# Optimization experiments

Hardware: AMD Instinct MI355X
Metric: run time of the kernel (lower is better)

## Reference

```python
import jax, jax.numpy as jnp
import numpy as np

# Module constants from Net.__init__
KS = (3, 8, 2)          # kernel_size per pseudo-coordinate dim
K = KS[0] * KS[1] * KS[2]  # 48 spline weight matrices per layer
DIM = 3
S = 2 ** DIM            # 8 nonzero degree-1 B-spline supports per edge
MAX_RADIUS = 4.5
N, E = 20000, 500000


def _glorot(key, shape):
    fan = shape[-2] + shape[-1]
    return jax.random.normal(key, shape, jnp.float32) * jnp.sqrt(2.0 / fan)


def setup_inputs() -> dict:
    key = jax.random.key(0)
    ks = jax.random.split(key, 12)
    x = jax.random.normal(ks[0], (N, 1), jnp.float32)
    edge_index = jax.random.randint(ks[1], (2, E), 0, N)
    # raw pseudo-coordinates in [0, max_radius); normalized inside reference
    pseudo = jax.random.uniform(ks[2], (E, DIM), jnp.float32) * MAX_RADIUS
    return {
        "x": x,
        "edge_index": edge_index,
        "pseudo": pseudo,
        "W1": _glorot(ks[3], (K, 1, 32)),   "root1": _glorot(ks[4], (1, 32)),   "b1": jnp.zeros((32,), jnp.float32),
        "W2": _glorot(ks[5], (K, 32, 64)),  "root2": _glorot(ks[6], (32, 64)),  "b2": jnp.zeros((64,), jnp.float32),
        "W3": _glorot(ks[7], (K, 64, 128)), "root3": _glorot(ks[8], (64, 128)), "b3": jnp.zeros((128,), jnp.float32),
    }


def spline_basis(u):
    """Degree-1 open B-spline basis. u: [E, DIM] in [0,1].
    Returns basis [E, S] and flat kernel indices kidx [E, S] into the K weights."""
    ks_f = jnp.array(KS, jnp.float32)
    pos = u * (ks_f - 1.0)                      # [E, DIM]
    lo = jnp.floor(pos)
    frac = pos - lo                             # interpolation weight per dim
    lo_i = lo.astype(jnp.int32)
    # all 2^DIM corner offsets
    bits = jnp.array([[(s >> d) & 1 for d in range(DIM)] for s in range(S)], jnp.int32)  # [S, DIM]
    idx = jnp.clip(lo_i[:, None, :] + bits[None, :, :], 0, jnp.array(KS, jnp.int32) - 1)  # [E, S, DIM]
    w = jnp.where(bits[None, :, :] == 1, frac[:, None, :], 1.0 - frac[:, None, :])        # [E, S, DIM]
    basis = jnp.prod(w, axis=-1)                # [E, S]
    strides = jnp.array([KS[1] * KS[2], KS[2], 1], jnp.int32)
    kidx = (idx * strides[None, None, :]).sum(-1)  # [E, S]
    return basis, kidx


def spline_conv(x, src, dst, basis, kidx, W, root, bias):
    """SplineGCN layer: gather source features, weight by spline basis,
    scatter-add into per-(node, kernel) buckets, then contract with the K
    kernel matrices. Equivalent to sum_e basis * (x_src @ W[kidx]) at dst."""
    c_in = x.shape[1]
    contrib = basis[:, :, None] * x[src][:, None, :]          # [E, S, c_in]
    flat = (dst[:, None] * K + kidx).reshape(-1)              # [E*S]
    acc = jax.ops.segment_sum(contrib.reshape(-1, c_in), flat, num_segments=N * K)
    acc = acc.reshape(N, K, c_in)                             # [N, K, c_in]
    return jnp.einsum('nki,kio->no', acc, W) + x @ root + bias


def reference(x, edge_index, pseudo, W1, root1, b1, W2, root2, b2, W3, root3, b3):
    u = jnp.clip(pseudo / MAX_RADIUS, 0.0, 1.0)
    basis, kidx = spline_basis(u)
    src, dst = edge_index[0], edge_index[1]
    h = jax.nn.relu(spline_conv(x, src, dst, basis, kidx, W1, root1, b1))
    h = jax.nn.relu(spline_conv(h, src, dst, basis, kidx, W2, root2, b2))
    h = jax.nn.relu(spline_conv(h, src, dst, basis, kidx, W3, root3, b3))
    return jax.nn.log_softmax(h, axis=-1)
```

## Files before the change

### kernel.cpp

```cpp
#include <hip/hip_runtime.h>
#include <hip/hip_bf16.h>

#define NN_NODES 20000
#define NE_EDGES 500000
#define KTOT 48
#define BTSTRIDE 40

typedef __bf16 bf16x8 __attribute__((ext_vector_type(8)));
typedef float f32x4 __attribute__((ext_vector_type(4)));

__device__ inline unsigned short bf16_rne(float x) {
    unsigned int u = __float_as_uint(x);
    u = (u + 0x7fffu + ((u >> 16) & 1u)) >> 16;
    return (unsigned short)u;
}

__global__ void zero_kernel(int* __restrict__ p, int n) {
    int i = blockIdx.x * 256 + threadIdx.x;
    if (i < n) p[i] = 0;
}

__global__ void count_kernel(const int* __restrict__ ei, int* __restrict__ counts) {
    int e = blockIdx.x * 256 + threadIdx.x;
    if (e < NE_EDGES) atomicAdd(&counts[ei[NE_EDGES + e]], 1);
}

__global__ void scan_kernel(const int* __restrict__ counts, int* __restrict__ row_start) {
    __shared__ int part[256];
    const int CH = (NN_NODES + 255) / 256;
    int t = threadIdx.x;
    int begin = t * CH;
    int end = begin + CH;
    if (end > NN_NODES) end = NN_NODES;
    int sum = 0;
    for (int i = begin; i < end && i < NN_NODES; ++i) sum += counts[i];
    part[t] = sum;
    __syncthreads();
    for (int off = 1; off < 256; off <<= 1) {
        int v = (t >= off) ? part[t - off] : 0;
        __syncthreads();
        part[t] += v;
        __syncthreads();
    }
    int run = (t == 0) ? 0 : part[t - 1];
    for (int i = begin; i < end && i < NN_NODES; ++i) {
        row_start[i] = run;
        run += counts[i];
    }
    if (t == 255) row_start[NN_NODES] = part[255];
}

__global__ void edge_prep_sorted(const float* __restrict__ pseudo, const int* __restrict__ ei,
                                 const int* __restrict__ row_start, int* __restrict__ cursor,
                                 int* __restrict__ srcs,
                                 unsigned short* __restrict__ bas8bf,
                                 unsigned char* __restrict__ kidb) {
    int e = blockIdx.x * 256 + threadIdx.x;
    if (e >= NE_EDGES) return;
    const int ksa[3] = {3, 8, 2};
    float frac[3];
    int id_lo[3], id_hi[3];
#pragma unroll
    for (int d = 0; d < 3; ++d) {
        float u = pseudo[e * 3 + d] * (1.0f / 4.5f);
        u = fminf(fmaxf(u, 0.0f), 1.0f);
        float pos = u * (float)(ksa[d] - 1);
        float fl = floorf(pos);
        int lo = (int)fl;
        frac[d] = pos - fl;
        id_lo[d] = lo;
        id_hi[d] = (lo + 1 <= ksa[d] - 1) ? lo + 1 : lo - 1;
    }
    int d0 = ei[NE_EDGES + e];
    int p = atomicAdd(&cursor[d0], 1);
    int j = row_start[d0] + p;
    srcs[j] = ei[e];
#pragma unroll
    for (int s = 0; s < 8; ++s) {
        float w = 1.0f;
        int k = 0;
        const int strides[3] = {16, 2, 1};
#pragma unroll
        for (int d = 0; d < 3; ++d) {
            int bit = (s >> d) & 1;
            k += (bit ? id_hi[d] : id_lo[d]) * strides[d];
            w *= bit ? frac[d] : (1.0f - frac[d]);
        }
        bas8bf[(size_t)j * 8 + s] = bf16_rne(w);
        kidb[(size_t)j * 8 + s] = (unsigned char)k;
    }
}

__global__ __launch_bounds__(256) void layer1_fused_kernel(
    const int* __restrict__ srcs, const unsigned short* __restrict__ bas8bf,
    const unsigned char* __restrict__ kidb, const int* __restrict__ row_start,
    const float* __restrict__ x, const float* __restrict__ W1,
    const float* __restrict__ root1, const float* __restrict__ b1,
    unsigned short* __restrict__ h1bf) {
    __shared__ float w1s[KTOT * 32];
    __shared__ float scopy[4][8 * 49];
    int tid = threadIdx.x;
    for (int l = tid; l < KTOT * 32; l += 256) w1s[l] = W1[l];
    int w = tid >> 6, lane = tid & 63;
    int n = blockIdx.x * 4 + w;
    bool act = n < NN_NODES;
    float* sc = &scopy[w][0];
    for (int l = lane; l < 8 * 49; l += 64) sc[l] = 0.0f;
    if (act) {
        int beg = row_start[n], end = row_start[n + 1];
        int es = lane >> 3;
        for (int jb = beg; jb < end; jb += 8) {
            int j = jb + es;
            if (j < end) {
                float b = __uint_as_float((unsigned)bas8bf[(size_t)jb * 8 + lane] << 16);
                int k = kidb[(size_t)jb * 8 + lane];
                float xv = x[srcs[j]];
                sc[es * 49 + k] += b * xv;
            }
        }
        if (lane < KTOT) {
            float a = 0.0f;
#pragma unroll
            for (int e = 0; e < 8; ++e) a += sc[e * 49 + lane];
            sc[lane] = a;
        }
    }
    __syncthreads();
    if (act && lane < 32) {
        float s = b1[lane] + x[n] * root1[lane];
#pragma unroll 8
        for (int k = 0; k < KTOT; ++k) s = fmaf(sc[k], w1s[k * 32 + lane], s);
        h1bf[n * 32 + lane] = bf16_rne(fmaxf(s, 0.0f));
    }
}

__global__ void pack_w_kernel(const float* __restrict__ W, const float* __restrict__ root,
                              int KK, int NN, int total, unsigned short* __restrict__ Wp) {
    int tid = blockIdx.x * 256 + threadIdx.x;
    if (tid >= total) return;
    int nct = NN >> 4;
    int l = tid & 63;
    int c = (tid >> 6) % nct;
    int t = tid / (64 * nct);
    int n = c * 16 + (l & 15);
    int kbase = t * 32 + ((l >> 4) << 3);
    unsigned short vals[8];
#pragma unroll
    for (int jj = 0; jj < 8; ++jj) {
        int k = kbase + jj;
        float v = (k < KK) ? W[(size_t)k * NN + n] : root[(size_t)(k - KK) * NN + n];
        vals[jj] = bf16_rne(v);
    }
    *(uint4*)&Wp[(size_t)tid * 8] = *(uint4*)vals;
}

#define NSTR2 1816
__global__ __launch_bounds__(1024) void fused_l2_kernel(
    const int* __restrict__ srcs, const unsigned short* __restrict__ bas8bf,
    const unsigned char* __restrict__ kidb, const int* __restrict__ row_start,
    const unsigned short* __restrict__ h1bf, const unsigned short* __restrict__ Wp2,
    const float* __restrict__ b2, unsigned short* __restrict__ h2bf) {
    __shared__ unsigned short Arows[16 * NSTR2];
    __shared__ unsigned short BtAll[16][KTOT * BTSTRIDE];
    float* Cst = (float*)&BtAll[0][0];
    int w = threadIdx.x >> 6, lane = threadIdx.x & 63;
    int q = lane >> 4, l15 = lane & 15;
    unsigned short* Bt = &BtAll[w][0];

    {
        int n = blockIdx.x * 16 + w;
        int beg = row_start[n], end = row_start[n + 1];
        int cnt = end - beg;
        f32x4 acc[3][2] = {};
        for (int c0 = 0; c0 < cnt; c0 += 32) {
            uint4 z = make_uint4(0, 0, 0, 0);
            for (int l = lane; l < (KTOT * BTSTRIDE) / 8; l += 64) ((uint4*)Bt)[l] = z;
#pragma unroll
            for (int it = 0; it < 4; ++it) {
                int idx = it * 64 + lane;
                int jj = idx >> 3, s = idx & 7;
                int j = c0 + jj;
                if (j < cnt) {
                    unsigned short b = bas8bf[(size_t)(beg + j) * 8 + s];
                    int k = kidb[(size_t)(beg + j) * 8 + s];
                    Bt[k * BTSTRIDE + jj] = b;
                }
            }
            int srcv[8];
#pragma unroll
            for (int j = 0; j < 8; ++j) {
                int jc = c0 + q * 8 + j;
                jc = (jc < cnt) ? jc : (cnt - 1);
                srcv[j] = srcs[beg + jc];
            }
            bf16x8 afr[3];
#pragma unroll
            for (int mt = 0; mt < 3; ++mt) {
                uint4 raw = *(const uint4*)&Bt[(mt * 16 + l15) * BTSTRIDE + q * 8];
                afr[mt] = __builtin_bit_cast(bf16x8, raw);
            }
#pragma unroll
            for (int nt = 0; nt < 2; ++nt) {
                unsigned int bw[4];
#pragma unroll
                for (int jp = 0; jp < 4; ++jp) {
                    unsigned int lo = h1bf[(size_t)srcv[2 * jp] * 32 + nt * 16 + l15];
                    unsigned int hi = h1bf[(size_t)srcv[2 * jp + 1] * 32 + nt * 16 + l15];
                    bw[jp] = lo | (hi << 16);
                }
                uint4 braw = make_uint4(bw[0], bw[1], bw[2], bw[3]);
                bf16x8 bfr = __builtin_bit_cast(bf16x8, braw);
#pragma unroll
                for (int mt = 0; mt < 3; ++mt)
                    acc[mt][nt] = __builtin_amdgcn_mfma_f32_16x16x32_bf16(
                        afr[mt], bfr, acc[mt][nt], 0, 0, 0);
            }
        }
        unsigned short* arow = &Arows[w * NSTR2];
#pragma unroll
        for (int mt = 0; mt < 3; ++mt)
#pragma unroll
            for (int nt = 0; nt < 2; ++nt)
#pragma unroll
                for (int r = 0; r < 4; ++r)
                    arow[(mt * 16 + q * 4 + r) * 36 + nt * 16 + l15] =
                        bf16_rne(acc[mt][nt][r]);
        if (lane < 32) arow[48 * 36 + lane] = h1bf[(size_t)n * 32 + lane];
    }
    __syncthreads();

    {
        int tile = w & 3;
        int kq = w >> 2;
        int t0 = (kq * 49) / 4, t1 = ((kq + 1) * 49) / 4;
        f32x4 cacc = {};
        const uint4* wpq = (const uint4*)Wp2;
        uint4 nb = wpq[((size_t)t0 * 4 + tile) * 64 + lane];
        for (int t = t0; t < t1; ++t) {
            uint4 cb = nb;
            int tn = (t + 1 < t1) ? t + 1 : t;
            nb = wpq[((size_t)tn * 4 + tile) * 64 + lane];
            bf16x8 af = __builtin_bit_cast(
                bf16x8, *(const uint4*)&Arows[l15 * NSTR2 + t * 36 + (q << 3)]);
            bf16x8 bfr = __builtin_bit_cast(bf16x8, cb);
            cacc = __builtin_amdgcn_mfma_f32_16x16x32_bf16(af, bfr, cacc, 0, 0, 0);
        }
        float* cpart = Cst + kq * (16 * 66);
#pragma unroll
        for (int r = 0; r < 4; ++r)
            cpart[(q * 4 + r) * 66 + tile * 16 + l15] = cacc[r];
    }
    __syncthreads();

    {
        int row = threadIdx.x >> 6;
        int col = threadIdx.x & 63;
        int idx = row * 66 + col;
        float v = Cst[idx] + Cst[16 * 66 + idx] + Cst[32 * 66 + idx] + Cst[48 * 66 + idx];
        v = fmaxf(v + b2[col], 0.0f);
        int n = blockIdx.x * 16 + row;
        h2bf[(size_t)n * 64 + col] = bf16_rne(v);
    }
}

#define ASTR 3160
__global__ __launch_bounds__(1024) void fused_l3_kernel(
    const int* __restrict__ srcs, const unsigned short* __restrict__ bas8bf,
    const unsigned char* __restrict__ kidb, const int* __restrict__ row_start,
    const unsigned short* __restrict__ h2bf, const unsigned short* __restrict__ Wp3,
    const float* __restrict__ b3, float* __restrict__ out) {
    __shared__ unsigned short Arows[16 * ASTR];
    __shared__ unsigned short BtAll[16][KTOT * BTSTRIDE];
    float* Cst = (float*)&BtAll[0][0];
    int w = threadIdx.x >> 6, lane = threadIdx.x & 63;
    int q = lane >> 4, l15 = lane & 15;
    unsigned short* Bt = &BtAll[w][0];

    {
        int n = blockIdx.x * 16 + w;
        int beg = row_start[n], end = row_start[n + 1];
        int cnt = end - beg;
        f32x4 acc[3][4] = {};
        for (int c0 = 0; c0 < cnt; c0 += 32) {
            uint4 z = make_uint4(0, 0, 0, 0);
            for (int l = lane; l < (KTOT * BTSTRIDE) / 8; l += 64) ((uint4*)Bt)[l] = z;
#pragma unroll
            for (int it = 0; it < 4; ++it) {
                int idx = it * 64 + lane;
                int jj = idx >> 3, s = idx & 7;
                int j = c0 + jj;
                if (j < cnt) {
                    unsigned short b = bas8bf[(size_t)(beg + j) * 8 + s];
                    int k = kidb[(size_t)(beg + j) * 8 + s];
                    Bt[k * BTSTRIDE + jj] = b;
                }
            }
            int srcv[8];
#pragma unroll
            for (int j = 0; j < 8; ++j) {
                int jc = c0 + q * 8 + j;
                jc = (jc < cnt) ? jc : (cnt - 1);
                srcv[j] = srcs[beg + jc];
            }
            bf16x8 afr[3];
#pragma unroll
            for (int mt = 0; mt < 3; ++mt) {
                uint4 raw = *(const uint4*)&Bt[(mt * 16 + l15) * BTSTRIDE + q * 8];
                afr[mt] = __builtin_bit_cast(bf16x8, raw);
            }
#pragma unroll
            for (int nt = 0; nt < 4; ++nt) {
                unsigned int bw[4];
#pragma unroll
                for (int jp = 0; jp < 4; ++jp) {
                    unsigned int lo = h2bf[(size_t)srcv[2 * jp] * 64 + nt * 16 + l15];
                    unsigned int hi = h2bf[(size_t)srcv[2 * jp + 1] * 64 + nt * 16 + l15];
                    bw[jp] = lo | (hi << 16);
                }
                uint4 braw = make_uint4(bw[0], bw[1], bw[2], bw[3]);
                bf16x8 bfr = __builtin_bit_cast(bf16x8, braw);
#pragma unroll
                for (int mt = 0; mt < 3; ++mt)
                    acc[mt][nt] = __builtin_amdgcn_mfma_f32_16x16x32_bf16(
                        afr[mt], bfr, acc[mt][nt], 0, 0, 0);
            }
        }
        unsigned short* arow = &Arows[w * ASTR];
#pragma unroll
        for (int mt = 0; mt < 3; ++mt)
#pragma unroll
            for (int nt = 0; nt < 4; ++nt)
#pragma unroll
                for (int r = 0; r < 4; ++r)
                    arow[(mt * 16 + q * 4 + r) * 64 + nt * 16 + l15] =
                        bf16_rne(acc[mt][nt][r]);
        arow[3072 + lane] = h2bf[(size_t)(blockIdx.x * 16 + w) * 64 + lane];
    }
    __syncthreads();

    {
        int tile = w & 7;
        int half = w >> 3;
        int t0 = half * 49, t1 = t0 + 49;
        f32x4 cacc = {};
        const uint4* wpq = (const uint4*)Wp3;
        uint4 nb = wpq[((size_t)t0 * 8 + tile) * 64 + lane];
        for (int t = t0; t < t1; ++t) {
            uint4 cb = nb;
            int tn = (t + 1 < t1) ? t + 1 : t;
            nb = wpq[((size_t)tn * 8 + tile) * 64 + lane];
            bf16x8 af = __builtin_bit_cast(
                bf16x8, *(const uint4*)&Arows[l15 * ASTR + t * 32 + (q << 3)]);
            bf16x8 bfr = __builtin_bit_cast(bf16x8, cb);
            cacc = __builtin_amdgcn_mfma_f32_16x16x32_bf16(af, bfr, cacc, 0, 0, 0);
        }
        float* chalf = Cst + half * (16 * 130);
#pragma unroll
        for (int r = 0; r < 4; ++r)
            chalf[(q * 4 + r) * 130 + tile * 16 + l15] = cacc[r];
    }
    __syncthreads();

    if (threadIdx.x < 256) {
        int row = threadIdx.x >> 4;
        int cb0 = threadIdx.x & 15;
        float v[8];
        float mx = -1e30f;
#pragma unroll
        for (int c = 0; c < 8; ++c) {
            int idx = row * 130 + cb0 + c * 16;
            float s = Cst[idx] + Cst[16 * 130 + idx] + b3[cb0 + c * 16];
            s = fmaxf(s, 0.0f);
            v[c] = s;
            mx = fmaxf(mx, s);
        }
#pragma unroll
        for (int off = 8; off > 0; off >>= 1) mx = fmaxf(mx, __shfl_xor(mx, off));
        float se = 0.0f;
#pragma unroll
        for (int c = 0; c < 8; ++c) se += expf(v[c] - mx);
#pragma unroll
        for (int off = 8; off > 0; off >>= 1) se += __shfl_xor(se, off);
        float lse = mx + logf(se);
        int n = blockIdx.x * 16 + row;
#pragma unroll
        for (int c = 0; c < 8; ++c)
            out[(size_t)n * 128 + cb0 + c * 16] = v[c] - lse;
    }
}

extern "C" void kernel_launch(void* const* d_in, const int* in_sizes, int n_in,
                              void* d_out, int out_size, void* d_ws, size_t ws_size,
                              hipStream_t stream) {
    const float* x = (const float*)d_in[0];
    const int* ei = (const int*)d_in[1];
    const float* pseudo = (const float*)d_in[2];
    const float* W1 = (const float*)d_in[3];
    const float* root1 = (const float*)d_in[4];
    const float* b1 = (const float*)d_in[5];
    const float* W2 = (const float*)d_in[6];
    const float* root2 = (const float*)d_in[7];
    const float* b2 = (const float*)d_in[8];
    const float* W3 = (const float*)d_in[9];
    const float* root3 = (const float*)d_in[10];
    const float* b3 = (const float*)d_in[11];
    float* out = (float*)d_out;
    char* ws = (char*)d_ws;

    const int N = NN_NODES, E = NE_EDGES;
    const int Kp2 = 49 * 32;
    const int Kp3 = 49 * 64;
    size_t off = 0;
    auto carve = [&](size_t bytes) {
        size_t p = off;
        off += (bytes + 255) & ~(size_t)255;
        return p;
    };
    int* counts = (int*)(ws + carve((size_t)N * 4 * 2));
    int* cursor = counts + N;
    int* row_start = (int*)(ws + carve((size_t)(N + 1) * 4));
    int* srcs = (int*)(ws + carve((size_t)E * 4));
    unsigned short* bas8bf = (unsigned short*)(ws + carve((size_t)E * 8 * 2));
    unsigned char* kidb = (unsigned char*)(ws + carve((size_t)E * 8));
    unsigned short* h1bf = (unsigned short*)(ws + carve((size_t)N * 32 * 2));
    unsigned short* h2bf = (unsigned short*)(ws + carve((size_t)N * 64 * 2));
    unsigned short* Wp2 = (unsigned short*)(ws + carve((size_t)Kp2 * 64 * 2));
    unsigned short* Wp3 = (unsigned short*)(ws + carve((size_t)Kp3 * 128 * 2));

    int egrid = (E + 255) / 256;

    zero_kernel<<<(2 * N + 255) / 256, 256, 0, stream>>>(counts, 2 * N);
    count_kernel<<<egrid, 256, 0, stream>>>(ei, counts);
    scan_kernel<<<1, 256, 0, stream>>>(counts, row_start);
    edge_prep_sorted<<<egrid, 256, 0, stream>>>(pseudo, ei, row_start, cursor,
                                                srcs, bas8bf, kidb);

    int tot2 = (Kp2 / 32) * (64 / 16) * 64;
    int tot3 = (Kp3 / 32) * (128 / 16) * 64;
    pack_w_kernel<<<(tot2 + 255) / 256, 256, 0, stream>>>(W2, root2, KTOT * 32, 64, tot2, Wp2);
    pack_w_kernel<<<(tot3 + 255) / 256, 256, 0, stream>>>(W3, root3, KTOT * 64, 128, tot3, Wp3);

    layer1_fused_kernel<<<(N + 3) / 4, 256, 0, stream>>>(srcs, bas8bf, kidb, row_start, x,
                                                         W1, root1, b1, h1bf);

    fused_l2_kernel<<<N / 16, 1024, 0, stream>>>(srcs, bas8bf, kidb, row_start,
                                                 h1bf, Wp2, b2, h2bf);

    fused_l3_kernel<<<N / 16, 1024, 0, stream>>>(srcs, bas8bf, kidb, row_start,
                                                 h2bf, Wp3, b3, out);
}
```

Baseline: 290.4 us.

## Group nodes by in-degree so each block handles similar-degree nodes

Adds a counting sort of nodes by in-degree (histogram, scan, scatter) to build a permutation. Layers 2 and 3 then assign each 16-node block nodes of similar degree, so waves within a block wait less on the busiest node at the barrier. The cost is three small extra kernel launches, an extra indirection, and less locality for the h2/out writes.

```diff
diff --git a/kernel.cpp b/kernel.cpp
--- a/kernel.cpp
+++ b/kernel.cpp
@@ -48,6 +48,35 @@
         run += counts[i];
     }
     if (t == 255) row_start[NN_NODES] = part[255];
+}
+
+__global__ void hist_kernel(const int* __restrict__ counts, int* __restrict__ hist) {
+    int n = blockIdx.x * 256 + threadIdx.x;
+    if (n < NN_NODES) atomicAdd(&hist[min(counts[n], 127)], 1);
+}
+
+__global__ void scan128_kernel(const int* __restrict__ hist, int* __restrict__ offs) {
+    __shared__ int tmp[128];
+    int t = threadIdx.x;
+    tmp[t] = hist[t];
+    __syncthreads();
+    for (int off = 1; off < 128; off <<= 1) {
+        int v = (t >= off) ? tmp[t - off] : 0;
+        __syncthreads();
+        tmp[t] += v;
+        __syncthreads();
+    }
+    offs[t] = tmp[t] - hist[t];
+}
+
+__global__ void scatter_perm_kernel(const int* __restrict__ counts, int* __restrict__ offs,
+                                    int* __restrict__ perm) {
+    int n = blockIdx.x * 256 + threadIdx.x;
+    if (n < NN_NODES) {
+        int d = min(counts[n], 127);
+        int r = atomicAdd(&offs[d], 1);
+        perm[r] = n;
+    }
 }
 
 __global__ void edge_prep_sorted(const float* __restrict__ pseudo, const int* __restrict__ ei,
@@ -158,6 +187,7 @@
 __global__ __launch_bounds__(1024) void fused_l2_kernel(
     const int* __restrict__ srcs, const unsigned short* __restrict__ bas8bf,
     const unsigned char* __restrict__ kidb, const int* __restrict__ row_start,
+    const int* __restrict__ perm,
     const unsigned short* __restrict__ h1bf, const unsigned short* __restrict__ Wp2,
     const float* __restrict__ b2, unsigned short* __restrict__ h2bf) {
     __shared__ unsigned short Arows[16 * NSTR2];
@@ -168,7 +198,7 @@
     unsigned short* Bt = &BtAll[w][0];
 
     {
-        int n = blockIdx.x * 16 + w;
+        int n = perm[blockIdx.x * 16 + w];
         int beg = row_start[n], end = row_start[n + 1];
         int cnt = end - beg;
         f32x4 acc[3][2] = {};
@@ -258,7 +288,7 @@
         int idx = row * 66 + col;
         float v = Cst[idx] + Cst[16 * 66 + idx] + Cst[32 * 66 + idx] + Cst[48 * 66 + idx];
         v = fmaxf(v + b2[col], 0.0f);
-        int n = blockIdx.x * 16 + row;
+        int n = perm[blockIdx.x * 16 + row];
         h2bf[(size_t)n * 64 + col] = bf16_rne(v);
     }
 }
@@ -267,6 +297,7 @@
 __global__ __launch_bounds__(1024) void fused_l3_kernel(
     const int* __restrict__ srcs, const unsigned short* __restrict__ bas8bf,
     const unsigned char* __restrict__ kidb, const int* __restrict__ row_start,
+    const int* __restrict__ perm,
     const unsigned short* __restrict__ h2bf, const unsigned short* __restrict__ Wp3,
     const float* __restrict__ b3, float* __restrict__ out) {
     __shared__ unsigned short Arows[16 * ASTR];
@@ -277,7 +308,7 @@
     unsigned short* Bt = &BtAll[w][0];
 
     {
-        int n = blockIdx.x * 16 + w;
+        int n = perm[blockIdx.x * 16 + w];
         int beg = row_start[n], end = row_start[n + 1];
         int cnt = end - beg;
         f32x4 acc[3][4] = {};
@@ -334,7 +365,7 @@
                 for (int r = 0; r < 4; ++r)
                     arow[(mt * 16 + q * 4 + r) * 64 + nt * 16 + l15] =
                         bf16_rne(acc[mt][nt][r]);
-        arow[3072 + lane] = h2bf[(size_t)(blockIdx.x * 16 + w) * 64 + lane];
+        arow[3072 + lane] = h2bf[(size_t)n * 64 + lane];
     }
     __syncthreads();
 
@@ -382,7 +413,7 @@
 #pragma unroll
         for (int off = 8; off > 0; off >>= 1) se += __shfl_xor(se, off);
         float lse = mx + logf(se);
-        int n = blockIdx.x * 16 + row;
+        int n = perm[blockIdx.x * 16 + row];
 #pragma unroll
         for (int c = 0; c < 8; ++c)
             out[(size_t)n * 128 + cb0 + c * 16] = v[c] - lse;
@@ -419,6 +450,9 @@
     int* counts = (int*)(ws + carve((size_t)N * 4 * 2));
     int* cursor = counts + N;
     int* row_start = (int*)(ws + carve((size_t)(N + 1) * 4));
+    int* hist = (int*)(ws + carve(256 * 4));
+    int* offs = hist + 128;
+    int* perm = (int*)(ws + carve((size_t)N * 4));
     int* srcs = (int*)(ws + carve((size_t)E * 4));
     unsigned short* bas8bf = (unsigned short*)(ws + carve((size_t)E * 8 * 2));
     unsigned char* kidb = (unsigned char*)(ws + carve((size_t)E * 8));
@@ -428,10 +462,15 @@
     unsigned short* Wp3 = (unsigned short*)(ws + carve((size_t)Kp3 * 128 * 2));
 
     int egrid = (E + 255) / 256;
+    int ngrid = (N + 255) / 256;
 
     zero_kernel<<<(2 * N + 255) / 256, 256, 0, stream>>>(counts, 2 * N);
+    zero_kernel<<<1, 256, 0, stream>>>(hist, 256);
     count_kernel<<<egrid, 256, 0, stream>>>(ei, counts);
     scan_kernel<<<1, 256, 0, stream>>>(counts, row_start);
+    hist_kernel<<<ngrid, 256, 0, stream>>>(counts, hist);
+    scan128_kernel<<<1, 128, 0, stream>>>(hist, offs);
+    scatter_perm_kernel<<<ngrid, 256, 0, stream>>>(counts, offs, perm);
     edge_prep_sorted<<<egrid, 256, 0, stream>>>(pseudo, ei, row_start, cursor,
                                                 srcs, bas8bf, kidb);
 
@@ -443,9 +482,9 @@
     layer1_fused_kernel<<<(N + 3) / 4, 256, 0, stream>>>(srcs, bas8bf, kidb, row_start, x,
                                                          W1, root1, b1, h1bf);
 
-    fused_l2_kernel<<<N / 16, 1024, 0, stream>>>(srcs, bas8bf, kidb, row_start,
+    fused_l2_kernel<<<N / 16, 1024, 0, stream>>>(srcs, bas8bf, kidb, row_start, perm,
                                                  h1bf, Wp2, b2, h2bf);
 
-    fused_l3_kernel<<<N / 16, 1024, 0, stream>>>(srcs, bas8bf, kidb, row_start,
+    fused_l3_kernel<<<N / 16, 1024, 0, stream>>>(srcs, bas8bf, kidb, row_start, perm,
                                                  h2bf, Wp3, b3, out);
 }
```

Result: slower. 403.7 us (+39.0%).
